# Kernel optimization log

Hardware: AMD Instinct MI355X
Metric: run time of the kernel (lower is better)

## Reference

```python
import jax, jax.numpy as jnp
import numpy as np

HID = 512
EMB = 768
TOP_K = 8
LN_EPS = 1e-5
NORM_EPS = 1e-12


def _mlp_ln(x, W1, b1, W2, b2, g, beta):
    # Linear -> ReLU -> Linear -> LayerNorm
    h = jax.nn.relu(x @ W1 + b1)
    h = h @ W2 + b2
    mu = jnp.mean(h, axis=-1, keepdims=True)
    var = jnp.var(h, axis=-1, keepdims=True)
    return (h - mu) * jax.lax.rsqrt(var + LN_EPS) * g + beta


def _l2norm(x):
    n = jnp.linalg.norm(x, axis=-1, keepdims=True)
    return x / jnp.maximum(n, NORM_EPS)


def setup_inputs() -> dict:
    key = jax.random.key(0)
    ks = jax.random.split(key, 12)
    s_in = 1.0 / np.sqrt(EMB)
    s_h = 1.0 / np.sqrt(HID)
    inp = {
        "query_embeddings": jax.random.normal(ks[0], (64, 32, EMB), jnp.float32),
        "doc_embeddings": jax.random.normal(ks[1], (50000, 16, EMB), jnp.float32),
        "qW1": jax.random.normal(ks[2], (EMB, HID), jnp.float32) * s_in,
        "qb1": jnp.zeros((HID,), jnp.float32),
        "qW2": jax.random.normal(ks[3], (HID, HID), jnp.float32) * s_h,
        "qb2": jnp.zeros((HID,), jnp.float32),
        "qg": jnp.ones((HID,), jnp.float32),
        "qbeta": jnp.zeros((HID,), jnp.float32),
        "dW1": jax.random.normal(ks[4], (EMB, HID), jnp.float32) * s_in,
        "db1": jnp.zeros((HID,), jnp.float32),
        "dW2": jax.random.normal(ks[5], (HID, HID), jnp.float32) * s_h,
        "db2": jnp.zeros((HID,), jnp.float32),
        "dg": jnp.ones((HID,), jnp.float32),
        "dbeta": jnp.zeros((HID,), jnp.float32),
        "pW": jax.random.normal(ks[6], (HID, HID), jnp.float32) * s_h,
        "pb": jnp.zeros((HID,), jnp.float32),
        "temperature": jnp.asarray(1.0, jnp.float32),
    }
    return inp


def reference(query_embeddings, doc_embeddings, qW1, qb1, qW2, qb2, qg, qbeta,
              dW1, db1, dW2, db2, dg, dbeta, pW, pb, temperature):
    # Mean-pool over token dims, encode with MLP+LayerNorm
    q_repr = _mlp_ln(query_embeddings.mean(axis=1), qW1, qb1, qW2, qb2, qg, qbeta)  # [B,H]
    d_repr = _mlp_ln(doc_embeddings.mean(axis=1), dW1, db1, dW2, db2, dg, dbeta)    # [N,H]
    q_norm = _l2norm(q_repr @ pW + pb)
    d_norm = _l2norm(d_repr @ pW + pb)
    scores = (q_norm @ d_norm.T) / temperature  # [B,N]
    top_k_scores, top_k_indices = jax.lax.top_k(scores, TOP_K)  # [B,K]
    retrieved_docs = doc_embeddings[top_k_indices]  # [B,K,doc_len,EMB]
    return top_k_scores, retrieved_docs
```

## Files before the change

kernel.cpp:

```cpp
#include <hip/hip_runtime.h>

#define NQ 64
#define ND 50000
#define QTOK 32
#define DTOK 16
#define EMB 768
#define HID 512

typedef short s16x8 __attribute__((ext_vector_type(8)));
typedef float f32x4 __attribute__((ext_vector_type(4)));

__device__ __forceinline__ unsigned short f2bf(float f) {
    union { float f; unsigned u; } x; x.f = f;
    unsigned r = x.u + 0x7fffu + ((x.u >> 16) & 1u);
    return (unsigned short)(r >> 16);
}
__device__ __forceinline__ float bf2f(unsigned short h) {
    union { unsigned u; float f; } x; x.u = ((unsigned)h) << 16;
    return x.f;
}
__device__ __forceinline__ unsigned packhi2(float a, float b) {
    return (unsigned)f2bf(a) | ((unsigned)f2bf(b) << 16);
}
__device__ __forceinline__ unsigned packlo2(float a, float b) {
    unsigned short ha = f2bf(a), hb = f2bf(b);
    return (unsigned)f2bf(a - bf2f(ha)) | ((unsigned)f2bf(b - bf2f(hb)) << 16);
}

__device__ __forceinline__ void gload_lds16(const void* g, void* l) {
    __builtin_amdgcn_global_load_lds(
        (const __attribute__((address_space(1))) void*)g,
        (__attribute__((address_space(3))) void*)l, 16, 0, 0);
}


__global__ void pool_kernel(const float* __restrict__ in, float* __restrict__ out, int T) {
    int r = blockIdx.x;
    int t = threadIdx.x;
    const float4* ip = (const float4*)in + (size_t)r * T * (EMB / 4);
    float4 acc = make_float4(0.f, 0.f, 0.f, 0.f);
    for (int i = 0; i < T; ++i) {
        float4 v = ip[(size_t)i * (EMB / 4) + t];
        acc.x += v.x; acc.y += v.y; acc.z += v.z; acc.w += v.w;
    }
    float s = 1.0f / (float)T;
    acc.x *= s; acc.y *= s; acc.z *= s; acc.w *= s;
    ((float4*)out)[(size_t)r * (EMB / 4) + t] = acc;
}

__global__ void pool_aug(const float* __restrict__ in, ushort* __restrict__ out) {
    int r = blockIdx.x, t = threadIdx.x;
    const float4* ip = (const float4*)in + (size_t)r * DTOK * (EMB / 4) + t;
    float4 a = make_float4(0.f, 0.f, 0.f, 0.f);
    #pragma unroll
    for (int i = 0; i < DTOK; ++i) {
        float4 v = ip[(size_t)i * (EMB / 4)];
        a.x += v.x; a.y += v.y; a.z += v.z; a.w += v.w;
    }
    const float s = 1.0f / (float)DTOK;
    float v0 = a.x * s, v1 = a.y * s, v2 = a.z * s, v3 = a.w * s;
    ushort* base = out + (size_t)r * (2 * EMB);
    *(uint2*)(base + t * 4)       = make_uint2(packhi2(v0, v1), packhi2(v2, v3));
    *(uint2*)(base + EMB + t * 4) = make_uint2(packlo2(v0, v1), packlo2(v2, v3));
}

__global__ void wconv(const float* __restrict__ W, ushort* __restrict__ Wp, int K) {
    int n = blockIdx.x;
    ushort* base = Wp + (size_t)n * 2 * K;
    for (int k = threadIdx.x; k < K; k += blockDim.x) {
        float v = W[(size_t)k * HID + n];
        unsigned short hi = f2bf(v);
        base[k]     = hi;
        base[K + k] = f2bf(v - bf2f(hi));
    }
}

template <int MODE>
__global__ __launch_bounds__(512) void mfma_gemm2(const ushort* __restrict__ A,
                                                  const ushort* __restrict__ B,
                                                  const float* __restrict__ bias,
                                                  void* __restrict__ out,
                                                  int M, int K) {
    __shared__ ushort As[128 * 64];
    __shared__ ushort Bs[256 * 64];
    const int Ks = 2 * K;
    const int bm = blockIdx.x * 128;
    const int bn = blockIdx.y * 256;
    const int tid = threadIdx.x;
    const int lane = tid & 63;
    const int wave = tid >> 6;
    const int wr = wave >> 2;
    const int wc = wave & 3;
    f32x4 acc[4][4] = {};

    for (int k0 = 0; k0 < 3 * K; k0 += 64) {
        const int ka = (k0 < 2 * K) ? k0 : k0 - 2 * K;
        const int kb = (k0 < K) ? k0 : k0 - K;
        #pragma unroll
        for (int c = 0; c < 2; ++c) {
            int idx = c * 512 + tid;
            int row = idx >> 3, s = idx & 7;
            int gr = bm + row; if (gr >= M) gr = M - 1;
            int ks = (s ^ (row & 7)) << 3;
            gload_lds16(A + (size_t)gr * Ks + ka + ks, As + idx * 8);
        }
        #pragma unroll
        for (int c = 0; c < 4; ++c) {
            int idx = c * 512 + tid;
            int n = idx >> 3, s = idx & 7;
            int ks = (s ^ (n & 7)) << 3;
            gload_lds16(B + (size_t)(bn + n) * Ks + kb + ks, Bs + idx * 8);
        }
        __syncthreads();

        #pragma unroll
        for (int kk = 0; kk < 2; ++kk) {
            const int sp = kk * 4 + (lane >> 4);
            s16x8 a[4], b[4];
            #pragma unroll
            for (int i = 0; i < 4; ++i) {
                int r = wr * 64 + i * 16 + (lane & 15);
                a[i] = *(const s16x8*)(As + r * 64 + ((sp ^ (r & 7)) << 3));
            }
            #pragma unroll
            for (int j = 0; j < 4; ++j) {
                int n = wc * 64 + j * 16 + (lane & 15);
                b[j] = *(const s16x8*)(Bs + n * 64 + ((sp ^ (n & 7)) << 3));
            }
            #pragma unroll
            for (int i = 0; i < 4; ++i)
                #pragma unroll
                for (int j = 0; j < 4; ++j)
                    acc[i][j] = __builtin_amdgcn_mfma_f32_16x16x32_bf16(a[i], b[j], acc[i][j], 0, 0, 0);
        }
        __syncthreads();
    }

    #pragma unroll
    for (int j = 0; j < 4; ++j) {
        int col = bn + wc * 64 + j * 16 + (lane & 15);
        float bv = bias[col];
        #pragma unroll
        for (int i = 0; i < 4; ++i) {
            #pragma unroll
            for (int r = 0; r < 4; ++r) {
                int grow = bm + wr * 64 + i * 16 + ((lane >> 4) << 2) + r;
                if (grow >= M) continue;
                float v = acc[i][j][r] + bv;
                if (MODE == 1) {
                    v = fmaxf(v, 0.0f);
                    unsigned short hi = f2bf(v);
                    ushort* op = (ushort*)out + (size_t)grow * (2 * HID);
                    op[col]       = hi;
                    op[HID + col] = f2bf(v - bf2f(hi));
                } else {
                    ((float*)out)[(size_t)grow * HID + col] = v;
                }
            }
        }
    }
}

__global__ __launch_bounds__(512) void mfma_scores(const ushort* __restrict__ A,
                                                   const ushort* __restrict__ B,
                                                   float* __restrict__ out,
                                                   int M, int N_B, int K, long ldo,
                                                   const float* __restrict__ temp) {
    __shared__ ushort As[128 * 64];
    __shared__ ushort Bs[256 * 64];
    const int Ks = 2 * K;
    const int bm = blockIdx.x * 128;
    const int bn = blockIdx.y * 256;
    const int tid = threadIdx.x;
    const int lane = tid & 63;
    const int wave = tid >> 6;
    const int wr = wave >> 2;
    const int wc = wave & 3;
    f32x4 acc[4][4] = {};

    for (int k0 = 0; k0 < 3 * K; k0 += 64) {
        const int ka = (k0 < 2 * K) ? k0 : k0 - 2 * K;
        const int kb = (k0 < K) ? k0 : k0 - K;
        #pragma unroll
        for (int c = 0; c < 2; ++c) {
            int idx = c * 512 + tid;
            int row = idx >> 3, s = idx & 7;
            int gr = bm + row; if (gr >= M) gr = M - 1;
            int ks = (s ^ (row & 7)) << 3;
            gload_lds16(A + (size_t)gr * Ks + ka + ks, As + idx * 8);
        }
        #pragma unroll
        for (int c = 0; c < 4; ++c) {
            int idx = c * 512 + tid;
            int n = idx >> 3, s = idx & 7;
            int gn = bn + n; if (gn >= N_B) gn = N_B - 1;
            int ks = (s ^ (n & 7)) << 3;
            gload_lds16(B + (size_t)gn * Ks + kb + ks, Bs + idx * 8);
        }
        __syncthreads();

        #pragma unroll
        for (int kk = 0; kk < 2; ++kk) {
            const int sp = kk * 4 + (lane >> 4);
            s16x8 a[4], b[4];
            #pragma unroll
            for (int i = 0; i < 4; ++i) {
                int r = wr * 64 + i * 16 + (lane & 15);
                a[i] = *(const s16x8*)(As + r * 64 + ((sp ^ (r & 7)) << 3));
            }
            #pragma unroll
            for (int j = 0; j < 4; ++j) {
                int n = wc * 64 + j * 16 + (lane & 15);
                b[j] = *(const s16x8*)(Bs + n * 64 + ((sp ^ (n & 7)) << 3));
            }
            #pragma unroll
            for (int i = 0; i < 4; ++i)
                #pragma unroll
                for (int j = 0; j < 4; ++j)
                    acc[i][j] = __builtin_amdgcn_mfma_f32_16x16x32_bf16(a[i], b[j], acc[i][j], 0, 0, 0);
        }
        __syncthreads();
    }

    float invT = 1.0f / temp[0];
    #pragma unroll
    for (int j = 0; j < 4; ++j) {
        int gcol = bn + wc * 64 + j * 16 + (lane & 15);
        #pragma unroll
        for (int i = 0; i < 4; ++i)
            #pragma unroll
            for (int r = 0; r < 4; ++r) {
                int grow = bm + wr * 64 + i * 16 + ((lane >> 4) << 2) + r;
                if (grow < M && gcol < N_B)
                    out[(size_t)grow * ldo + gcol] = acc[i][j][r] * invT;
            }
    }
}

__global__ __launch_bounds__(256) void ln_kernel(float* __restrict__ x,
                                                 const float* __restrict__ g,
                                                 const float* __restrict__ be, int M) {
    int wv = threadIdx.x >> 6, lane = threadIdx.x & 63;
    int row = blockIdx.x * 4 + wv;
    if (row >= M) return;
    float4* p = (float4*)(x + (size_t)row * HID);
    float4 a = p[lane * 2], b = p[lane * 2 + 1];
    float s  = a.x + a.y + a.z + a.w + b.x + b.y + b.z + b.w;
    float sq = a.x*a.x + a.y*a.y + a.z*a.z + a.w*a.w
             + b.x*b.x + b.y*b.y + b.z*b.z + b.w*b.w;
    #pragma unroll
    for (int o = 32; o > 0; o >>= 1) { s += __shfl_xor(s, o); sq += __shfl_xor(sq, o); }
    float mu  = s * (1.0f / HID);
    float var = sq * (1.0f / HID) - mu * mu;
    float r   = rsqrtf(var + 1e-5f);
    const float4* gp = (const float4*)g;
    const float4* bp = (const float4*)be;
    float4 g0 = gp[lane * 2], g1 = gp[lane * 2 + 1];
    float4 b0 = bp[lane * 2], b1 = bp[lane * 2 + 1];
    a.x = (a.x - mu) * r * g0.x + b0.x;  a.y = (a.y - mu) * r * g0.y + b0.y;
    a.z = (a.z - mu) * r * g0.z + b0.z;  a.w = (a.w - mu) * r * g0.w + b0.w;
    b.x = (b.x - mu) * r * g1.x + b1.x;  b.y = (b.y - mu) * r * g1.y + b1.y;
    b.z = (b.z - mu) * r * g1.z + b1.z;  b.w = (b.w - mu) * r * g1.w + b1.w;
    p[lane * 2] = a; p[lane * 2 + 1] = b;
}

__device__ __forceinline__ void store_hilo(ushort* __restrict__ base, int lane,
                                           float v0, float v1, float v2, float v3,
                                           float v4, float v5, float v6, float v7) {
    *(uint4*)(base + lane * 8) =
        make_uint4(packhi2(v0, v1), packhi2(v2, v3), packhi2(v4, v5), packhi2(v6, v7));
    *(uint4*)(base + HID + lane * 8) =
        make_uint4(packlo2(v0, v1), packlo2(v2, v3), packlo2(v4, v5), packlo2(v6, v7));
}

__global__ __launch_bounds__(256) void ln_aug(const float* __restrict__ x,
                                              const float* __restrict__ g,
                                              const float* __restrict__ be,
                                              ushort* __restrict__ out, int M) {
    int wv = threadIdx.x >> 6, lane = threadIdx.x & 63;
    int row = blockIdx.x * 4 + wv;
    if (row >= M) return;
    const float4* p = (const float4*)(x + (size_t)row * HID);
    float4 a = p[lane * 2], b = p[lane * 2 + 1];
    float s  = a.x + a.y + a.z + a.w + b.x + b.y + b.z + b.w;
    float sq = a.x*a.x + a.y*a.y + a.z*a.z + a.w*a.w
             + b.x*b.x + b.y*b.y + b.z*b.z + b.w*b.w;
    #pragma unroll
    for (int o = 32; o > 0; o >>= 1) { s += __shfl_xor(s, o); sq += __shfl_xor(sq, o); }
    float mu  = s * (1.0f / HID);
    float var = sq * (1.0f / HID) - mu * mu;
    float r   = rsqrtf(var + 1e-5f);
    const float4* gp = (const float4*)g;
    const float4* bp = (const float4*)be;
    float4 g0 = gp[lane * 2], g1 = gp[lane * 2 + 1];
    float4 b0 = bp[lane * 2], b1 = bp[lane * 2 + 1];
    store_hilo(out + (size_t)row * (2 * HID), lane,
               (a.x - mu) * r * g0.x + b0.x, (a.y - mu) * r * g0.y + b0.y,
               (a.z - mu) * r * g0.z + b0.z, (a.w - mu) * r * g0.w + b0.w,
               (b.x - mu) * r * g1.x + b1.x, (b.y - mu) * r * g1.y + b1.y,
               (b.z - mu) * r * g1.z + b1.z, (b.w - mu) * r * g1.w + b1.w);
}

__global__ __launch_bounds__(256) void l2_aug(const float* __restrict__ x,
                                              ushort* __restrict__ out, int M) {
    int wv = threadIdx.x >> 6, lane = threadIdx.x & 63;
    int row = blockIdx.x * 4 + wv;
    if (row >= M) return;
    const float4* p = (const float4*)(x + (size_t)row * HID);
    float4 a = p[lane * 2], b = p[lane * 2 + 1];
    float sq = a.x*a.x + a.y*a.y + a.z*a.z + a.w*a.w
             + b.x*b.x + b.y*b.y + b.z*b.z + b.w*b.w;
    #pragma unroll
    for (int o = 32; o > 0; o >>= 1) sq += __shfl_xor(sq, o);
    float n = sqrtf(sq);
    float r = 1.0f / fmaxf(n, 1e-12f);
    store_hilo(out + (size_t)row * (2 * HID), lane,
               a.x * r, a.y * r, a.z * r, a.w * r,
               b.x * r, b.y * r, b.z * r, b.w * r);
}

__global__ __launch_bounds__(256) void l2_kernel(float* __restrict__ x, int M) {
    int wv = threadIdx.x >> 6, lane = threadIdx.x & 63;
    int row = blockIdx.x * 4 + wv;
    if (row >= M) return;
    float4* p = (float4*)(x + (size_t)row * HID);
    float4 a = p[lane * 2], b = p[lane * 2 + 1];
    float sq = a.x*a.x + a.y*a.y + a.z*a.z + a.w*a.w
             + b.x*b.x + b.y*b.y + b.z*b.z + b.w*b.w;
    #pragma unroll
    for (int o = 32; o > 0; o >>= 1) sq += __shfl_xor(sq, o);
    float n = sqrtf(sq);
    float r = 1.0f / fmaxf(n, 1e-12f);
    a.x *= r; a.y *= r; a.z *= r; a.w *= r;
    b.x *= r; b.y *= r; b.z *= r; b.w *= r;
    p[lane * 2] = a; p[lane * 2 + 1] = b;
}

__global__ __launch_bounds__(256) void fp32_aug(const float* __restrict__ x,
                                                ushort* __restrict__ out, int M) {
    int wv = threadIdx.x >> 6, lane = threadIdx.x & 63;
    int row = blockIdx.x * 4 + wv;
    if (row >= M) return;
    const float4* p = (const float4*)(x + (size_t)row * HID);
    float4 a = p[lane * 2], b = p[lane * 2 + 1];
    store_hilo(out + (size_t)row * (2 * HID), lane,
               a.x, a.y, a.z, a.w, b.x, b.y, b.z, b.w);
}

template <int RELU>
__global__ __launch_bounds__(256) void gemm_nn(const float* __restrict__ A,
                                               const float* __restrict__ W,
                                               const float* __restrict__ bias,
                                               float* __restrict__ C,
                                               int M, int K, int N) {
    __shared__ float As[16][68];
    __shared__ float Bs[16][64];
    const int bm = blockIdx.x * 64;
    const int bn = blockIdx.y * 64;
    const int tid = threadIdx.x;
    const int tx = tid & 15, ty = tid >> 4;
    float acc[4][4] = {};
    for (int k0 = 0; k0 < K; k0 += 16) {
        {
            int row = tid >> 2;
            int kk  = (tid & 3) << 2;
            int gr  = bm + row;
            float4 v = make_float4(0.f, 0.f, 0.f, 0.f);
            if (gr < M) v = *(const float4*)(A + (size_t)gr * K + k0 + kk);
            As[kk + 0][row] = v.x; As[kk + 1][row] = v.y;
            As[kk + 2][row] = v.z; As[kk + 3][row] = v.w;
        }
        {
            int n  = tid & 63;
            int kb = tid >> 6;
            #pragma unroll
            for (int q = 0; q < 4; ++q) {
                int kr = kb + q * 4;
                Bs[kr][n] = W[(size_t)(k0 + kr) * N + bn + n];
            }
        }
        __syncthreads();
        #pragma unroll
        for (int k = 0; k < 16; ++k) {
            float4 av = *(const float4*)&As[k][ty << 2];
            float4 bv = *(const float4*)&Bs[k][tx << 2];
            float a[4] = {av.x, av.y, av.z, av.w};
            float b[4] = {bv.x, bv.y, bv.z, bv.w};
            #pragma unroll
            for (int i = 0; i < 4; ++i)
                #pragma unroll
                for (int j = 0; j < 4; ++j)
                    acc[i][j] = fmaf(a[i], b[j], acc[i][j]);
        }
        __syncthreads();
    }
    #pragma unroll
    for (int i = 0; i < 4; ++i) {
        int gr = bm + (ty << 2) + i;
        if (gr >= M) continue;
        #pragma unroll
        for (int j = 0; j < 4; ++j) {
            int gc = bn + (tx << 2) + j;
            float v = acc[i][j] + bias[gc];
            if (RELU) v = fmaxf(v, 0.0f);
            C[(size_t)gr * N + gc] = v;
        }
    }
}

__global__ __launch_bounds__(256) void topk_kernel(const float* __restrict__ scores,
                                                   float* __restrict__ out_scores,
                                                   int* __restrict__ out_idx, int N) {
    __shared__ float ls[2048];
    __shared__ int   li[2048];
    const int q   = blockIdx.x;
    const int tid = threadIdx.x;
    const float* row = scores + (size_t)q * N;
    float s[8]; int ix[8];
    #pragma unroll
    for (int i = 0; i < 8; ++i) { s[i] = -1e30f; ix[i] = 0x7fffffff; }
    for (int j = tid; j < N; j += 256) {
        float v = row[j];
        if (v > s[7]) {
            s[7] = v; ix[7] = j;
            #pragma unroll
            for (int t = 7; t > 0; --t) {
                bool sw = (s[t] > s[t-1]) || (s[t] == s[t-1] && ix[t] < ix[t-1]);
                if (sw) {
                    float tv = s[t]; s[t] = s[t-1]; s[t-1] = tv;
                    int   ti = ix[t]; ix[t] = ix[t-1]; ix[t-1] = ti;
                }
            }
        }
    }
    #pragma unroll
    for (int i = 0; i < 8; ++i) { ls[tid * 8 + i] = s[i]; li[tid * 8 + i] = ix[i]; }
    __syncthreads();
    for (int w = 64; w >= 1; w >>= 2) {
        if (tid < w) {
            #pragma unroll
            for (int i = 0; i < 8; ++i) { s[i] = -1e30f; ix[i] = 0x7fffffff; }
            #pragma unroll
            for (int c = 0; c < 32; ++c) {
                float v  = ls[tid * 32 + c];
                int   vi = li[tid * 32 + c];
                bool better = (v > s[7]) || (v == s[7] && vi < ix[7]);
                if (better) {
                    s[7] = v; ix[7] = vi;
                    #pragma unroll
                    for (int t = 7; t > 0; --t) {
                        bool sw = (s[t] > s[t-1]) || (s[t] == s[t-1] && ix[t] < ix[t-1]);
                        if (sw) {
                            float tv = s[t]; s[t] = s[t-1]; s[t-1] = tv;
                            int   ti = ix[t]; ix[t] = ix[t-1]; ix[t-1] = ti;
                        }
                    }
                }
            }
        }
        __syncthreads();
        if (tid < w) {
            #pragma unroll
            for (int i = 0; i < 8; ++i) { ls[tid * 8 + i] = s[i]; li[tid * 8 + i] = ix[i]; }
        }
        __syncthreads();
    }
    if (tid < 8) {
        out_scores[(size_t)q * 8 + tid] = ls[tid];
        out_idx[q * 8 + tid]            = li[tid];
    }
}

__global__ __launch_bounds__(256) void gather_kernel(const float* __restrict__ docs,
                                                     const int* __restrict__ idx,
                                                     float* __restrict__ out) {
    const int b = blockIdx.x;
    const int d = idx[b];
    const float4* src = (const float4*)(docs + (size_t)d * DTOK * EMB);
    float4*       dst = (float4*)(out + (size_t)b * DTOK * EMB);
    for (int i = threadIdx.x; i < DTOK * EMB / 4; i += 256) dst[i] = src[i];
}

extern "C" void kernel_launch(void* const* d_in, const int* in_sizes, int n_in,
                              void* d_out, int out_size, void* d_ws, size_t ws_size,
                              hipStream_t stream) {
    const float* qe   = (const float*)d_in[0];
    const float* de   = (const float*)d_in[1];
    const float* qW1  = (const float*)d_in[2];
    const float* qb1  = (const float*)d_in[3];
    const float* qW2  = (const float*)d_in[4];
    const float* qb2  = (const float*)d_in[5];
    const float* qg   = (const float*)d_in[6];
    const float* qbe  = (const float*)d_in[7];
    const float* dW1  = (const float*)d_in[8];
    const float* db1  = (const float*)d_in[9];
    const float* dW2  = (const float*)d_in[10];
    const float* db2  = (const float*)d_in[11];
    const float* dg   = (const float*)d_in[12];
    const float* dbe  = (const float*)d_in[13];
    const float* pW   = (const float*)d_in[14];
    const float* pb   = (const float*)d_in[15];
    const float* temp = (const float*)d_in[16];

    float* out = (float*)d_out;

    char* w = (char*)d_ws;
    float*  scores = (float*)w;                 w += (size_t)NQ * ND * 4;
    ushort* W1p    = (ushort*)w;                w += (size_t)HID * 2 * EMB * 2;
    ushort* W2p    = (ushort*)w;                w += (size_t)HID * 2 * HID * 2;
    ushort* pWp    = (ushort*)w;                w += (size_t)HID * 2 * HID * 2;
    float*  qpool  = (float*)w;                 w += (size_t)NQ * EMB * 4;
    float*  qh1    = (float*)w;                 w += (size_t)NQ * HID * 4;
    float*  qh2    = (float*)w;                 w += (size_t)NQ * HID * 4;
    float*  qn     = (float*)w;                 w += (size_t)NQ * HID * 4;
    ushort* qaug   = (ushort*)w;                w += (size_t)NQ * 2 * HID * 2;
    int*    tidx   = (int*)w;                   w += 4096;
    ushort* pooled = (ushort*)w;                w += (size_t)ND * 2 * EMB * 2;
    ushort* h1a    = (ushort*)w;                w += (size_t)ND * 2 * HID * 2;
    float*  h2     = (float*)w;                 w += (size_t)ND * HID * 4;
    ushort* lna    = pooled;
    float*  pproj  = h2;
    ushort* Daug   = h1a;

    const int GM = (ND + 127) / 128;

    wconv<<<HID, 256, 0, stream>>>(dW1, W1p, EMB);
    wconv<<<HID, 256, 0, stream>>>(dW2, W2p, HID);
    wconv<<<HID, 256, 0, stream>>>(pW,  pWp, HID);

    pool_kernel<<<NQ, 192, 0, stream>>>(qe, qpool, QTOK);
    gemm_nn<1><<<dim3(1, 8), 256, 0, stream>>>(qpool, qW1, qb1, qh1, NQ, EMB, HID);
    gemm_nn<0><<<dim3(1, 8), 256, 0, stream>>>(qh1, qW2, qb2, qh2, NQ, HID, HID);
    ln_kernel<<<(NQ + 3) / 4, 256, 0, stream>>>(qh2, qg, qbe, NQ);
    gemm_nn<0><<<dim3(1, 8), 256, 0, stream>>>(qh2, pW, pb, qn, NQ, HID, HID);
    l2_kernel<<<(NQ + 3) / 4, 256, 0, stream>>>(qn, NQ);
    fp32_aug<<<(NQ + 3) / 4, 256, 0, stream>>>(qn, qaug, NQ);

    pool_aug<<<ND, 192, 0, stream>>>(de, pooled);
    mfma_gemm2<1><<<dim3(GM, 2), 512, 0, stream>>>(pooled, W1p, db1, h1a, ND, EMB);
    mfma_gemm2<0><<<dim3(GM, 2), 512, 0, stream>>>(h1a, W2p, db2, h2, ND, HID);
    ln_aug<<<(ND + 3) / 4, 256, 0, stream>>>(h2, dg, dbe, lna, ND);
    mfma_gemm2<0><<<dim3(GM, 2), 512, 0, stream>>>(lna, pWp, pb, pproj, ND, HID);
    l2_aug<<<(ND + 3) / 4, 256, 0, stream>>>(pproj, Daug, ND);

    mfma_scores<<<dim3(1, (ND + 255) / 256), 512, 0, stream>>>(qaug, Daug, scores,
                                                               NQ, ND, HID, (long)ND, temp);

    topk_kernel<<<NQ, 256, 0, stream>>>(scores, out, tidx, ND);
    gather_kernel<<<NQ * 8, 256, 0, stream>>>(de, tidx, out + NQ * 8);
}
```

Measured before the change: 1.452 ms.

## Merge query encoder path into batched document MFMA pipeline

The query pooling, MLP, LayerNorm, projection and L2 steps now run as extra rows of the document pipeline. Query rows are appended after a padded document block so the MFMA GEMMs, LN and L2 kernels select query or document weights per tile. This removes seven small serial launches, including slow fp32 SIMT GEMMs, at the cost of one extra row tile and two more weight conversions. Launch bounds also gain a minimum-occupancy hint of 4.

```diff
diff --git a/kernel.cpp b/kernel.cpp
--- a/kernel.cpp
+++ b/kernel.cpp
@@ -2,6 +2,8 @@
 
 #define NQ 64
 #define ND 50000
+#define NDP 50048
+#define MT (NDP + NQ)
 #define QTOK 32
 #define DTOK 16
 #define EMB 768
@@ -34,32 +36,23 @@
 }
 
 
-__global__ void pool_kernel(const float* __restrict__ in, float* __restrict__ out, int T) {
-    int r = blockIdx.x;
-    int t = threadIdx.x;
-    const float4* ip = (const float4*)in + (size_t)r * T * (EMB / 4);
-    float4 acc = make_float4(0.f, 0.f, 0.f, 0.f);
+__global__ void pool_aug_all(const float* __restrict__ de, const float* __restrict__ qe,
+                             ushort* __restrict__ out) {
+    int blk = blockIdx.x, t = threadIdx.x;
+    const float* src;
+    int T;
+    size_t orow;
+    if (blk < ND) { src = de + (size_t)blk * DTOK * EMB; T = DTOK; orow = blk; }
+    else          { int qr = blk - ND; src = qe + (size_t)qr * QTOK * EMB; T = QTOK; orow = NDP + qr; }
+    const float4* ip = (const float4*)src + t;
+    float4 a = make_float4(0.f, 0.f, 0.f, 0.f);
     for (int i = 0; i < T; ++i) {
-        float4 v = ip[(size_t)i * (EMB / 4) + t];
-        acc.x += v.x; acc.y += v.y; acc.z += v.z; acc.w += v.w;
-    }
-    float s = 1.0f / (float)T;
-    acc.x *= s; acc.y *= s; acc.z *= s; acc.w *= s;
-    ((float4*)out)[(size_t)r * (EMB / 4) + t] = acc;
-}
-
-__global__ void pool_aug(const float* __restrict__ in, ushort* __restrict__ out) {
-    int r = blockIdx.x, t = threadIdx.x;
-    const float4* ip = (const float4*)in + (size_t)r * DTOK * (EMB / 4) + t;
-    float4 a = make_float4(0.f, 0.f, 0.f, 0.f);
-    #pragma unroll
-    for (int i = 0; i < DTOK; ++i) {
         float4 v = ip[(size_t)i * (EMB / 4)];
         a.x += v.x; a.y += v.y; a.z += v.z; a.w += v.w;
     }
-    const float s = 1.0f / (float)DTOK;
+    const float s = 1.0f / (float)T;
     float v0 = a.x * s, v1 = a.y * s, v2 = a.z * s, v3 = a.w * s;
-    ushort* base = out + (size_t)r * (2 * EMB);
+    ushort* base = out + orow * (2 * EMB);
     *(uint2*)(base + t * 4)       = make_uint2(packhi2(v0, v1), packhi2(v2, v3));
     *(uint2*)(base + EMB + t * 4) = make_uint2(packlo2(v0, v1), packlo2(v2, v3));
 }
@@ -76,16 +69,21 @@
 }
 
 template <int MODE>
-__global__ __launch_bounds__(512) void mfma_gemm2(const ushort* __restrict__ A,
-                                                  const ushort* __restrict__ B,
-                                                  const float* __restrict__ bias,
-                                                  void* __restrict__ out,
-                                                  int M, int K) {
+__global__ __launch_bounds__(512, 4) void mfma_gemm2(const ushort* __restrict__ A,
+                                                     const ushort* __restrict__ Bd,
+                                                     const ushort* __restrict__ Bq,
+                                                     const float* __restrict__ biasd,
+                                                     const float* __restrict__ biasq,
+                                                     void* __restrict__ out,
+                                                     int M, int K) {
     __shared__ ushort As[128 * 64];
     __shared__ ushort Bs[256 * 64];
     const int Ks = 2 * K;
     const int bm = blockIdx.x * 128;
     const int bn = blockIdx.y * 256;
+    const bool isq = (bm >= NDP);
+    const ushort* B = isq ? Bq : Bd;
+    const float* bias = isq ? biasq : biasd;
     const int tid = threadIdx.x;
     const int lane = tid & 63;
     const int wave = tid >> 6;
@@ -161,11 +159,11 @@
     }
 }
 
-__global__ __launch_bounds__(512) void mfma_scores(const ushort* __restrict__ A,
-                                                   const ushort* __restrict__ B,
-                                                   float* __restrict__ out,
-                                                   int M, int N_B, int K, long ldo,
-                                                   const float* __restrict__ temp) {
+__global__ __launch_bounds__(512, 4) void mfma_scores(const ushort* __restrict__ A,
+                                                      const ushort* __restrict__ B,
+                                                      float* __restrict__ out,
+                                                      int M, int N_B, int K, long ldo,
+                                                      const float* __restrict__ temp) {
     __shared__ ushort As[128 * 64];
     __shared__ ushort Bs[256 * 64];
     const int Ks = 2 * K;
@@ -237,33 +235,6 @@
     }
 }
 
-__global__ __launch_bounds__(256) void ln_kernel(float* __restrict__ x,
-                                                 const float* __restrict__ g,
-                                                 const float* __restrict__ be, int M) {
-    int wv = threadIdx.x >> 6, lane = threadIdx.x & 63;
-    int row = blockIdx.x * 4 + wv;
-    if (row >= M) return;
-    float4* p = (float4*)(x + (size_t)row * HID);
-    float4 a = p[lane * 2], b = p[lane * 2 + 1];
-    float s  = a.x + a.y + a.z + a.w + b.x + b.y + b.z + b.w;
-    float sq = a.x*a.x + a.y*a.y + a.z*a.z + a.w*a.w
-             + b.x*b.x + b.y*b.y + b.z*b.z + b.w*b.w;
-    #pragma unroll
-    for (int o = 32; o > 0; o >>= 1) { s += __shfl_xor(s, o); sq += __shfl_xor(sq, o); }
-    float mu  = s * (1.0f / HID);
-    float var = sq * (1.0f / HID) - mu * mu;
-    float r   = rsqrtf(var + 1e-5f);
-    const float4* gp = (const float4*)g;
-    const float4* bp = (const float4*)be;
-    float4 g0 = gp[lane * 2], g1 = gp[lane * 2 + 1];
-    float4 b0 = bp[lane * 2], b1 = bp[lane * 2 + 1];
-    a.x = (a.x - mu) * r * g0.x + b0.x;  a.y = (a.y - mu) * r * g0.y + b0.y;
-    a.z = (a.z - mu) * r * g0.z + b0.z;  a.w = (a.w - mu) * r * g0.w + b0.w;
-    b.x = (b.x - mu) * r * g1.x + b1.x;  b.y = (b.y - mu) * r * g1.y + b1.y;
-    b.z = (b.z - mu) * r * g1.z + b1.z;  b.w = (b.w - mu) * r * g1.w + b1.w;
-    p[lane * 2] = a; p[lane * 2 + 1] = b;
-}
-
 __device__ __forceinline__ void store_hilo(ushort* __restrict__ base, int lane,
                                            float v0, float v1, float v2, float v3,
                                            float v4, float v5, float v6, float v7) {
@@ -274,12 +245,16 @@
 }
 
 __global__ __launch_bounds__(256) void ln_aug(const float* __restrict__ x,
-                                              const float* __restrict__ g,
-                                              const float* __restrict__ be,
+                                              const float* __restrict__ dg,
+                                              const float* __restrict__ dbe,
+                                              const float* __restrict__ qg,
+                                              const float* __restrict__ qbe,
                                               ushort* __restrict__ out, int M) {
     int wv = threadIdx.x >> 6, lane = threadIdx.x & 63;
     int row = blockIdx.x * 4 + wv;
     if (row >= M) return;
+    const float* g  = (row >= NDP) ? qg  : dg;
+    const float* be = (row >= NDP) ? qbe : dbe;
     const float4* p = (const float4*)(x + (size_t)row * HID);
     float4 a = p[lane * 2], b = p[lane * 2 + 1];
     float s  = a.x + a.y + a.z + a.w + b.x + b.y + b.z + b.w;
@@ -317,95 +292,6 @@
     store_hilo(out + (size_t)row * (2 * HID), lane,
                a.x * r, a.y * r, a.z * r, a.w * r,
                b.x * r, b.y * r, b.z * r, b.w * r);
-}
-
-__global__ __launch_bounds__(256) void l2_kernel(float* __restrict__ x, int M) {
-    int wv = threadIdx.x >> 6, lane = threadIdx.x & 63;
-    int row = blockIdx.x * 4 + wv;
-    if (row >= M) return;
-    float4* p = (float4*)(x + (size_t)row * HID);
-    float4 a = p[lane * 2], b = p[lane * 2 + 1];
-    float sq = a.x*a.x + a.y*a.y + a.z*a.z + a.w*a.w
-             + b.x*b.x + b.y*b.y + b.z*b.z + b.w*b.w;
-    #pragma unroll
-    for (int o = 32; o > 0; o >>= 1) sq += __shfl_xor(sq, o);
-    float n = sqrtf(sq);
-    float r = 1.0f / fmaxf(n, 1e-12f);
-    a.x *= r; a.y *= r; a.z *= r; a.w *= r;
-    b.x *= r; b.y *= r; b.z *= r; b.w *= r;
-    p[lane * 2] = a; p[lane * 2 + 1] = b;
-}
-
-__global__ __launch_bounds__(256) void fp32_aug(const float* __restrict__ x,
-                                                ushort* __restrict__ out, int M) {
-    int wv = threadIdx.x >> 6, lane = threadIdx.x & 63;
-    int row = blockIdx.x * 4 + wv;
-    if (row >= M) return;
-    const float4* p = (const float4*)(x + (size_t)row * HID);
-    float4 a = p[lane * 2], b = p[lane * 2 + 1];
-    store_hilo(out + (size_t)row * (2 * HID), lane,
-               a.x, a.y, a.z, a.w, b.x, b.y, b.z, b.w);
-}
-
-template <int RELU>
-__global__ __launch_bounds__(256) void gemm_nn(const float* __restrict__ A,
-                                               const float* __restrict__ W,
-                                               const float* __restrict__ bias,
-                                               float* __restrict__ C,
-                                               int M, int K, int N) {
-    __shared__ float As[16][68];
-    __shared__ float Bs[16][64];
-    const int bm = blockIdx.x * 64;
-    const int bn = blockIdx.y * 64;
-    const int tid = threadIdx.x;
-    const int tx = tid & 15, ty = tid >> 4;
-    float acc[4][4] = {};
-    for (int k0 = 0; k0 < K; k0 += 16) {
-        {
-            int row = tid >> 2;
-            int kk  = (tid & 3) << 2;
-            int gr  = bm + row;
-            float4 v = make_float4(0.f, 0.f, 0.f, 0.f);
-            if (gr < M) v = *(const float4*)(A + (size_t)gr * K + k0 + kk);
-            As[kk + 0][row] = v.x; As[kk + 1][row] = v.y;
-            As[kk + 2][row] = v.z; As[kk + 3][row] = v.w;
-        }
-        {
-            int n  = tid & 63;
-            int kb = tid >> 6;
-            #pragma unroll
-            for (int q = 0; q < 4; ++q) {
-                int kr = kb + q * 4;
-                Bs[kr][n] = W[(size_t)(k0 + kr) * N + bn + n];
-            }
-        }
-        __syncthreads();
-        #pragma unroll
-        for (int k = 0; k < 16; ++k) {
-            float4 av = *(const float4*)&As[k][ty << 2];
-            float4 bv = *(const float4*)&Bs[k][tx << 2];
-            float a[4] = {av.x, av.y, av.z, av.w};
-            float b[4] = {bv.x, bv.y, bv.z, bv.w};
-            #pragma unroll
-            for (int i = 0; i < 4; ++i)
-                #pragma unroll
-                for (int j = 0; j < 4; ++j)
-                    acc[i][j] = fmaf(a[i], b[j], acc[i][j]);
-        }
-        __syncthreads();
-    }
-    #pragma unroll
-    for (int i = 0; i < 4; ++i) {
-        int gr = bm + (ty << 2) + i;
-        if (gr >= M) continue;
-        #pragma unroll
-        for (int j = 0; j < 4; ++j) {
-            int gc = bn + (tx << 2) + j;
-            float v = acc[i][j] + bias[gc];
-            if (RELU) v = fmaxf(v, 0.0f);
-            C[(size_t)gr * N + gc] = v;
-        }
-    }
 }
 
 __global__ __launch_bounds__(256) void topk_kernel(const float* __restrict__ scores,
@@ -509,39 +395,31 @@
     ushort* W1p    = (ushort*)w;                w += (size_t)HID * 2 * EMB * 2;
     ushort* W2p    = (ushort*)w;                w += (size_t)HID * 2 * HID * 2;
     ushort* pWp    = (ushort*)w;                w += (size_t)HID * 2 * HID * 2;
-    float*  qpool  = (float*)w;                 w += (size_t)NQ * EMB * 4;
-    float*  qh1    = (float*)w;                 w += (size_t)NQ * HID * 4;
-    float*  qh2    = (float*)w;                 w += (size_t)NQ * HID * 4;
-    float*  qn     = (float*)w;                 w += (size_t)NQ * HID * 4;
-    ushort* qaug   = (ushort*)w;                w += (size_t)NQ * 2 * HID * 2;
+    ushort* QW1p   = (ushort*)w;                w += (size_t)HID * 2 * EMB * 2;
+    ushort* QW2p   = (ushort*)w;                w += (size_t)HID * 2 * HID * 2;
     int*    tidx   = (int*)w;                   w += 4096;
-    ushort* pooled = (ushort*)w;                w += (size_t)ND * 2 * EMB * 2;
-    ushort* h1a    = (ushort*)w;                w += (size_t)ND * 2 * HID * 2;
-    float*  h2     = (float*)w;                 w += (size_t)ND * HID * 4;
+    ushort* pooled = (ushort*)w;                w += (size_t)MT * 2 * EMB * 2;
+    ushort* h1a    = (ushort*)w;                w += (size_t)MT * 2 * HID * 2;
+    float*  h2     = (float*)w;                 w += (size_t)MT * HID * 4;
     ushort* lna    = pooled;
     float*  pproj  = h2;
     ushort* Daug   = h1a;
-
-    const int GM = (ND + 127) / 128;
+    ushort* qaug   = Daug + (size_t)NDP * 2 * HID;
+
+    const int GM = (MT + 127) / 128;
 
     wconv<<<HID, 256, 0, stream>>>(dW1, W1p, EMB);
     wconv<<<HID, 256, 0, stream>>>(dW2, W2p, HID);
     wconv<<<HID, 256, 0, stream>>>(pW,  pWp, HID);
-
-    pool_kernel<<<NQ, 192, 0, stream>>>(qe, qpool, QTOK);
-    gemm_nn<1><<<dim3(1, 8), 256, 0, stream>>>(qpool, qW1, qb1, qh1, NQ, EMB, HID);
-    gemm_nn<0><<<dim3(1, 8), 256, 0, stream>>>(qh1, qW2, qb2, qh2, NQ, HID, HID);
-    ln_kernel<<<(NQ + 3) / 4, 256, 0, stream>>>(qh2, qg, qbe, NQ);
-    gemm_nn<0><<<dim3(1, 8), 256, 0, stream>>>(qh2, pW, pb, qn, NQ, HID, HID);
-    l2_kernel<<<(NQ + 3) / 4, 256, 0, stream>>>(qn, NQ);
-    fp32_aug<<<(NQ + 3) / 4, 256, 0, stream>>>(qn, qaug, NQ);
-
-    pool_aug<<<ND, 192, 0, stream>>>(de, pooled);
-    mfma_gemm2<1><<<dim3(GM, 2), 512, 0, stream>>>(pooled, W1p, db1, h1a, ND, EMB);
-    mfma_gemm2<0><<<dim3(GM, 2), 512, 0, stream>>>(h1a, W2p, db2, h2, ND, HID);
-    ln_aug<<<(ND + 3) / 4, 256, 0, stream>>>(h2, dg, dbe, lna, ND);
-    mfma_gemm2<0><<<dim3(GM, 2), 512, 0, stream>>>(lna, pWp, pb, pproj, ND, HID);
-    l2_aug<<<(ND + 3) / 4, 256, 0, stream>>>(pproj, Daug, ND);
+    wconv<<<HID, 256, 0, stream>>>(qW1, QW1p, EMB);
+    wconv<<<HID, 256, 0, stream>>>(qW2, QW2p, HID);
+
+    pool_aug_all<<<ND + NQ, 192, 0, stream>>>(de, qe, pooled);
+    mfma_gemm2<1><<<dim3(GM, 2), 512, 0, stream>>>(pooled, W1p, QW1p, db1, qb1, h1a, MT, EMB);
+    mfma_gemm2<0><<<dim3(GM, 2), 512, 0, stream>>>(h1a, W2p, QW2p, db2, qb2, h2, MT, HID);
+    ln_aug<<<(MT + 3) / 4, 256, 0, stream>>>(h2, dg, dbe, qg, qbe, lna, MT);
+    mfma_gemm2<0><<<dim3(GM, 2), 512, 0, stream>>>(lna, pWp, pWp, pb, pb, pproj, MT, HID);
+    l2_aug<<<(MT + 3) / 4, 256, 0, stream>>>(pproj, Daug, MT);
 
     mfma_scores<<<dim3(1, (ND + 255) / 256), 512, 0, stream>>>(qaug, Daug, scores,
                                                                NQ, ND, HID, (long)ND, temp);
```

Measured after the change: 1.353 ms. -6.8%, faster.
